# Optimization experiments

Measured on AMD Instinct MI355X. Metric: run time of the kernel, lower is better.

## Reference

```python
import jax, jax.numpy as jnp
import numpy as np

NH = 16      # num_heads
D = 128      # head_dim
C = 64       # chunk_size
EPS = 1e-12  # F.normalize eps


def setup_inputs() -> dict:
    key = jax.random.key(0)
    ks = jax.random.split(key, 12)
    B, L, H = 4, 4096, 2048
    std = 0.02
    f32 = jnp.float32
    inp = {
        "hidden_states": jax.random.normal(ks[0], (B, L, H), f32),
        # torch nn.Linear weights are [out_features, in_features]
        "q_w": jax.random.normal(ks[1], (NH * D, H), f32) * std,
        "q_b": jnp.zeros((NH * D,), f32),
        "k_w": jax.random.normal(ks[2], (NH * D, H), f32) * std,
        "k_b": jnp.zeros((NH * D,), f32),
        "v_w": jax.random.normal(ks[3], (NH * D, H), f32) * std,
        "v_b": jnp.zeros((NH * D,), f32),
        "a_w": jax.random.normal(ks[4], (NH, H), f32) * std,
        "a_b": jnp.zeros((NH,), f32),
        "b_w": jax.random.normal(ks[5], (NH, H), f32) * std,
        "b_b": jnp.zeros((NH,), f32),
        "og_w": jax.random.normal(ks[6], (NH * D, H), f32) * std,  # no bias
        "o_w": jax.random.normal(ks[7], (H, NH * D), f32) * std,
        "o_b": jnp.zeros((H,), f32),
    }
    return inp


def _l2norm(x):
    n = jnp.linalg.norm(x, axis=-1, keepdims=True)
    return x / jnp.maximum(n, EPS)


def reference(hidden_states, q_w, q_b, k_w, k_b, v_w, v_b,
              a_w, a_b, b_w, b_b, og_w, o_w, o_b):
    B, L, H = hidden_states.shape
    nh, d, c = NH, D, C
    hs = hidden_states

    q = (hs @ q_w.T + q_b).reshape(B, L, nh, d)
    k = (hs @ k_w.T + k_b).reshape(B, L, nh, d)
    v = (hs @ v_w.T + v_b).reshape(B, L, nh, d)
    # alpha = sigmoid(hs @ a_w.T + a_b) is computed in the original module but
    # never affects the output (alpha_mean / log_alpha are dead code) -> omitted.
    beta = jax.nn.softplus(hs @ b_w.T + b_b)            # [B,L,nh]

    scale = float(d) ** 0.5
    qn = _l2norm(q / scale)                              # normalize makes /scale moot, kept faithful
    kn = _l2norm(k / scale)
    gv = beta[..., None] * v                             # [B,L,nh,d]

    nchunks = L // c

    def to_chunks(x):  # [B,L,nh,d] -> [B,nchunks,nh,c,d]
        return x.reshape(B, nchunks, c, nh, d).transpose(0, 1, 3, 2, 4)

    qc, kc, gvc = to_chunks(qn), to_chunks(kn), to_chunks(gv)

    attn = jnp.einsum('bnhid,bnhjd->bnhij', qc, kc)      # per-chunk QK^T
    pos = jnp.arange(c, dtype=jnp.float32)
    dist = jnp.clip(pos[None, :] - pos[:, None], 0.0, None)   # (j-i) clamped >=0
    decay = jnp.exp(-0.1 * dist)
    causal = pos[None, :] <= pos[:, None]                # keep j<=i, zero j>i
    mask = jnp.where(causal, decay, 0.0)                 # [c,c]
    out = jnp.einsum('bnhij,bnhjd->bnhid', attn * mask, gvc)

    out = out.transpose(0, 1, 3, 2, 4).reshape(B, L, nh * d)
    gate = jax.nn.silu(hs @ og_w.T)                      # output_gate has no bias
    out = out * gate
    return out @ o_w.T + o_b
```

## Files before the change

kernel.cpp:

```cpp
#include <hip/hip_runtime.h>


typedef __bf16 bf16x8 __attribute__((ext_vector_type(8)));
typedef float f32x4 __attribute__((ext_vector_type(4)));

typedef __attribute__((address_space(1))) const unsigned int g_u32;
typedef __attribute__((address_space(3))) unsigned int l_u32;

__device__ __forceinline__ void cp16(const unsigned short* g, unsigned short* l) {
  __builtin_amdgcn_global_load_lds((g_u32*)g, (l_u32*)l, 16, 0, 0);
}

__device__ __forceinline__ unsigned short f2bf(float x) {
  unsigned u = __builtin_bit_cast(unsigned, x);
  u += 0x7fffu + ((u >> 16) & 1u);
  return (unsigned short)(u >> 16);
}
__device__ __forceinline__ float bf2f(unsigned short h) {
  return __builtin_bit_cast(float, (unsigned)h << 16);
}
__device__ __forceinline__ unsigned pk2(float a, float b) {
  return (unsigned)f2bf(a) | ((unsigned)f2bf(b) << 16);
}

__global__ __launch_bounds__(256) void cvt_bf16(const float* __restrict__ in,
                                                unsigned short* __restrict__ out,
                                                int n) {
  int i = (blockIdx.x * 256 + threadIdx.x) * 8;
  if (i >= n) return;
  float4 f0 = *(const float4*)(in + i);
  float4 f1 = *(const float4*)(in + i + 4);
  uint4 u;
  u.x = pk2(f0.x, f0.y); u.y = pk2(f0.z, f0.w);
  u.z = pk2(f1.x, f1.y); u.w = pk2(f1.z, f1.w);
  *(uint4*)(out + i) = u;
}

__global__ __launch_bounds__(256) void build_bias(
    const float* __restrict__ qb, const float* __restrict__ kb,
    const float* __restrict__ vb, float* __restrict__ bias_cat) {
  int i = blockIdx.x * 256 + threadIdx.x;
  float v = 0.f;
  if (i < 2048) v = qb[i];
  else if (i < 4096) v = kb[i - 2048];
  else if (i < 6144) v = vb[i - 4096];
  bias_cat[i] = v;
}

__global__ __launch_bounds__(256) void beta_kernel(
    const float* __restrict__ hs, const float* __restrict__ bw,
    const float* __restrict__ bb, float* __restrict__ beta,
    unsigned short* __restrict__ hsb) {
  __shared__ float row[2048];
  __shared__ float part[16][17];
  const int m = blockIdx.x;
  const float* src = hs + (size_t)m * 2048;
  for (int i = threadIdx.x; i < 512; i += 256)
    ((float4*)row)[i] = ((const float4*)src)[i];
  __syncthreads();
  if (hsb) {
    int e = threadIdx.x * 8;
    uint4 u;
    u.x = pk2(row[e], row[e + 1]);     u.y = pk2(row[e + 2], row[e + 3]);
    u.z = pk2(row[e + 4], row[e + 5]); u.w = pk2(row[e + 6], row[e + 7]);
    *(uint4*)(hsb + (size_t)m * 2048 + e) = u;
  }
  const int h = threadIdx.x >> 4, j = threadIdx.x & 15;
  const float* w = bw + h * 2048;
  float s = 0.f;
  #pragma unroll 8
  for (int kk = 0; kk < 128; kk++) {
    int k = j + (kk << 4);
    s += row[k] * w[k];
  }
  part[h][j] = s;
  __syncthreads();
  if (threadIdx.x < 16) {
    int hh = threadIdx.x;
    float t = bb[hh];
    #pragma unroll
    for (int j2 = 0; j2 < 16; j2++) t += part[hh][j2];
    beta[(size_t)m * 16 + hh] = fmaxf(t, 0.f) + log1pf(__expf(-fabsf(t)));
  }
}

template <int EPI, int N, int K>
__global__ __launch_bounds__(512, 2) void gemm256(
    const unsigned short* __restrict__ A, const unsigned short* __restrict__ Bw,
    const float* __restrict__ bias, const float* __restrict__ beta,
    void* __restrict__ Cv) {
  constexpr int NT = K / 32;
  __shared__ __align__(16) unsigned short As[4 * 8192];
  __shared__ __align__(16) unsigned short Bs[4 * 8192];
  const int tid = threadIdx.x;
  const int m0 = blockIdx.y * 256;
  const int n0 = blockIdx.x * 256;
  const int wid = tid >> 6, lane = tid & 63;
  const int wm = wid >> 2, wn = wid & 3;
  const int quad = lane >> 4, l16 = lane & 15;

  const int trow = tid >> 2;
  const int tch = (((tid & 3) ^ ((trow >> 1) & 3)) << 3);
  const unsigned short* Ag = A + (size_t)(m0 + trow) * K + tch;
  const unsigned short* Bg = Bw + (size_t)(n0 + trow) * K + tch;

  const int chs = ((quad ^ ((l16 >> 1) & 3)) << 4);
  const int a_lane = (wm * 128 + l16) * 64 + chs;
  const int b_lane = (wn * 64 + l16) * 64 + chs;

  f32x4 acc[8][4] = {};

  #pragma unroll
  for (int tt = 0; tt < 3; ++tt) {
    const size_t kk = (size_t)tt * 32;
    unsigned short* la = As + tt * 8192 + tid * 8;
    unsigned short* lb = Bs + tt * 8192 + tid * 8;
    cp16(Ag + kk, la);
    cp16(Ag + (size_t)128 * K + kk, la + 4096);
    cp16(Bg + kk, lb);
    cp16(Bg + (size_t)128 * K + kk, lb + 4096);
  }
  asm volatile("s_waitcnt vmcnt(8)" ::: "memory");
  __builtin_amdgcn_s_barrier();

  for (int t = 0; t < NT; ++t) {
    const int cur = t & 3;
    const int nb = (t + 3) & 3;
    const size_t k3 = (size_t)((t + 3 < NT) ? (t + 3) : (NT - 1)) * 32;
    const char* At = (const char*)As + cur * 16384 + a_lane;
    const char* Bt = (const char*)Bs + cur * 16384 + b_lane;
    unsigned short* la = As + nb * 8192 + tid * 8;
    unsigned short* lb = Bs + nb * 8192 + tid * 8;

    bf16x8 af[4], bfr[4];

    #pragma unroll
    for (int mi = 0; mi < 4; mi++) af[mi] = *(const bf16x8*)(At + mi * 1024);
    #pragma unroll
    for (int ni = 0; ni < 4; ni++) bfr[ni] = *(const bf16x8*)(Bt + ni * 1024);
    cp16(Ag + k3, la);
    cp16(Ag + (size_t)128 * K + k3, la + 4096);
    __builtin_amdgcn_s_barrier();
    asm volatile("s_waitcnt lgkmcnt(0)" ::: "memory");
    __builtin_amdgcn_s_setprio(1);
    #pragma unroll
    for (int mi = 0; mi < 4; mi++)
      #pragma unroll
      for (int ni = 0; ni < 4; ni++)
        acc[mi][ni] = __builtin_amdgcn_mfma_f32_16x16x32_bf16(
            af[mi], bfr[ni], acc[mi][ni], 0, 0, 0);
    __builtin_amdgcn_s_setprio(0);
    __builtin_amdgcn_s_barrier();

    #pragma unroll
    for (int mi = 0; mi < 4; mi++) af[mi] = *(const bf16x8*)(At + (4 + mi) * 1024);
    cp16(Bg + k3, lb);
    cp16(Bg + (size_t)128 * K + k3, lb + 4096);
    __builtin_amdgcn_s_barrier();
    asm volatile("s_waitcnt lgkmcnt(0)" ::: "memory");
    __builtin_amdgcn_s_setprio(1);
    #pragma unroll
    for (int mi = 0; mi < 4; mi++)
      #pragma unroll
      for (int ni = 0; ni < 4; ni++)
        acc[4 + mi][ni] = __builtin_amdgcn_mfma_f32_16x16x32_bf16(
            af[mi], bfr[ni], acc[4 + mi][ni], 0, 0, 0);
    __builtin_amdgcn_s_setprio(0);

    if (t != NT - 1) {
      asm volatile("s_waitcnt vmcnt(8)" ::: "memory");
      __builtin_amdgcn_s_barrier();
    }
  }
  asm volatile("s_waitcnt vmcnt(0)" ::: "memory");

  if (EPI == 0) {
    const int mode = n0 >> 11;
    unsigned short* outp =
        (unsigned short*)Cv + (size_t)mode * ((size_t)16384 * 2048);
    const int head = ((n0 + wn * 64) >> 7) & 15;
    #pragma unroll
    for (int mi = 0; mi < 8; mi++) {
      #pragma unroll
      for (int r = 0; r < 4; r++) {
        const int row = m0 + wm * 128 + mi * 16 + quad * 4 + r;
        const float bsc = (mode == 2) ? beta[(size_t)row * 16 + head] : 1.f;
        #pragma unroll
        for (int ni = 0; ni < 4; ni++) {
          const int col = n0 + wn * 64 + ni * 16 + l16;
          float x = acc[mi][ni][r] + bias[col];
          if (mode == 2) x *= bsc;
          if (mode == 3) x = x / (1.f + __expf(-x));
          outp[(size_t)row * 2048 + (col & 2047)] = f2bf(x);
        }
      }
    }
  } else {
    #pragma unroll
    for (int mi = 0; mi < 8; mi++)
      #pragma unroll
      for (int r = 0; r < 4; r++) {
        const int row = m0 + wm * 128 + mi * 16 + quad * 4 + r;
        #pragma unroll
        for (int ni = 0; ni < 4; ni++) {
          const int col = n0 + wn * 64 + ni * 16 + l16;
          ((float*)Cv)[(size_t)row * N + col] = acc[mi][ni][r] + bias[col];
        }
      }
  }
}

constexpr int GLDW = 40;
template <int EPI, bool ABF16>
__global__ __launch_bounds__(256) void gemm_bt(
    const void* __restrict__ Av, const float* __restrict__ Bw,
    const float* __restrict__ bias, const float* __restrict__ beta,
    void* __restrict__ Cv, int M, int N, int K) {
  __shared__ unsigned short As[128 * GLDW];
  __shared__ unsigned short Bs[128 * GLDW];
  const int tid = threadIdx.x;
  const int m0 = blockIdx.y * 128;
  const int n0 = blockIdx.x * 128;
  const int wid = tid >> 6, lane = tid & 63;
  const int wm = wid >> 1, wn = wid & 1;
  const int quad = lane >> 4, l16 = lane & 15;
  const int srow = tid >> 1, skh = (tid & 1) << 4;

  f32x4 acc[4][4] = {};
  const float* Bg = Bw + (size_t)(n0 + srow) * K + skh;

  for (int kb = 0; kb < K; kb += 32) {
    if (ABF16) {
      const unsigned short* Ag =
          (const unsigned short*)Av + (size_t)(m0 + srow) * K + kb + skh;
      uint4 u0 = ((const uint4*)Ag)[0];
      uint4 u1 = ((const uint4*)Ag)[1];
      uint4* d = (uint4*)&As[srow * GLDW + skh];
      d[0] = u0; d[1] = u1;
    } else {
      const float* Ag = (const float*)Av + (size_t)(m0 + srow) * K + kb + skh;
      float4 f0 = ((const float4*)Ag)[0];
      float4 f1 = ((const float4*)Ag)[1];
      float4 f2 = ((const float4*)Ag)[2];
      float4 f3 = ((const float4*)Ag)[3];
      unsigned* d = (unsigned*)&As[srow * GLDW + skh];
      d[0] = pk2(f0.x, f0.y); d[1] = pk2(f0.z, f0.w);
      d[2] = pk2(f1.x, f1.y); d[3] = pk2(f1.z, f1.w);
      d[4] = pk2(f2.x, f2.y); d[5] = pk2(f2.z, f2.w);
      d[6] = pk2(f3.x, f3.y); d[7] = pk2(f3.z, f3.w);
    }
    {
      const float* Bgk = Bg + kb;
      float4 f0 = ((const float4*)Bgk)[0];
      float4 f1 = ((const float4*)Bgk)[1];
      float4 f2 = ((const float4*)Bgk)[2];
      float4 f3 = ((const float4*)Bgk)[3];
      unsigned* d = (unsigned*)&Bs[srow * GLDW + skh];
      d[0] = pk2(f0.x, f0.y); d[1] = pk2(f0.z, f0.w);
      d[2] = pk2(f1.x, f1.y); d[3] = pk2(f1.z, f1.w);
      d[4] = pk2(f2.x, f2.y); d[5] = pk2(f2.z, f2.w);
      d[6] = pk2(f3.x, f3.y); d[7] = pk2(f3.z, f3.w);
    }
    __syncthreads();
    bf16x8 af[4], bfr[4];
    #pragma unroll
    for (int mi = 0; mi < 4; mi++)
      af[mi] = *(const bf16x8*)&As[(wm * 64 + mi * 16 + l16) * GLDW + (quad << 3)];
    #pragma unroll
    for (int ni = 0; ni < 4; ni++)
      bfr[ni] = *(const bf16x8*)&Bs[(wn * 64 + ni * 16 + l16) * GLDW + (quad << 3)];
    #pragma unroll
    for (int mi = 0; mi < 4; mi++)
      #pragma unroll
      for (int ni = 0; ni < 4; ni++)
        acc[mi][ni] = __builtin_amdgcn_mfma_f32_16x16x32_bf16(
            af[mi], bfr[ni], acc[mi][ni], 0, 0, 0);
    __syncthreads();
  }

  #pragma unroll
  for (int mi = 0; mi < 4; mi++) {
    #pragma unroll
    for (int r = 0; r < 4; r++) {
      const int row = m0 + wm * 64 + mi * 16 + quad * 4 + r;
      float bsc = 1.f;
      if (EPI == 1) bsc = beta[(size_t)row * 16 + blockIdx.x];
      #pragma unroll
      for (int ni = 0; ni < 4; ni++) {
        const int col = n0 + wn * 64 + ni * 16 + l16;
        float x = acc[mi][ni][r];
        if (EPI != 2) x += bias[col];
        if (EPI == 1) x *= bsc;
        if (EPI == 2) x = x / (1.f + __expf(-x));
        if (EPI == 3)
          ((float*)Cv)[(size_t)row * N + col] = x;
        else
          ((unsigned short*)Cv)[(size_t)row * N + col] = f2bf(x);
      }
    }
  }
}

constexpr int QK_LDW = 132;
constexpr int GT_LDW = 66;
constexpr int SS_LDW = 68;

__global__ __launch_bounds__(256) void attn_kernel(
    const unsigned short* __restrict__ qn, const unsigned short* __restrict__ kn,
    const unsigned short* __restrict__ gvp, const unsigned short* __restrict__ gate,
    unsigned short* __restrict__ y) {
  __shared__ unsigned short qs[64 * QK_LDW];
  __shared__ unsigned short ks[64 * QK_LDW];
  __shared__ unsigned short gst[128 * GT_LDW];
  __shared__ unsigned short Ss[64 * SS_LDW];

  const int tid = threadIdx.x;
  const int m0 = blockIdx.x * 64;
  const int h = blockIdx.y;
  const size_t gbase = (size_t)m0 * 2048 + (size_t)h * 128;

  #pragma unroll
  for (int it = 0; it < 4; it++) {
    int e = tid + it * 256;
    int i = e >> 4;
    int c = (e & 15) << 3;
    size_t g = gbase + (size_t)i * 2048 + c;
    *(uint4*)&qs[i * QK_LDW + c] = *(const uint4*)&qn[g];
    *(uint4*)&ks[i * QK_LDW + c] = *(const uint4*)&kn[g];
    uint4 gvv = *(const uint4*)&gvp[g];
    unsigned short tmp[8];
    *(uint4*)tmp = gvv;
    #pragma unroll
    for (int t = 0; t < 8; t++) gst[(c + t) * GT_LDW + i] = tmp[t];
  }
  __syncthreads();

  {
    const int rr = tid >> 2;
    const int seg = (tid & 3) * 32;
    float ssq = 0.f, ssk = 0.f;
    #pragma unroll
    for (int k2 = 0; k2 < 32; k2 += 2) {
      unsigned uq = *(const unsigned*)&qs[rr * QK_LDW + seg + k2];
      unsigned uk = *(const unsigned*)&ks[rr * QK_LDW + seg + k2];
      float a = bf2f((unsigned short)(uq & 0xffff)), b = bf2f((unsigned short)(uq >> 16));
      float c2 = bf2f((unsigned short)(uk & 0xffff)), d2 = bf2f((unsigned short)(uk >> 16));
      ssq += a * a + b * b;
      ssk += c2 * c2 + d2 * d2;
    }
    ssq += __shfl_xor(ssq, 1); ssq += __shfl_xor(ssq, 2);
    ssk += __shfl_xor(ssk, 1); ssk += __shfl_xor(ssk, 2);
    float iq = rsqrtf(fmaxf(ssq, 1e-24f));
    float ik = rsqrtf(fmaxf(ssk, 1e-24f));
    #pragma unroll
    for (int k2 = 0; k2 < 32; k2 += 2) {
      unsigned uq = *(const unsigned*)&qs[rr * QK_LDW + seg + k2];
      unsigned uk = *(const unsigned*)&ks[rr * QK_LDW + seg + k2];
      float a = bf2f((unsigned short)(uq & 0xffff)), b = bf2f((unsigned short)(uq >> 16));
      float c2 = bf2f((unsigned short)(uk & 0xffff)), d2 = bf2f((unsigned short)(uk >> 16));
      *(unsigned*)&qs[rr * QK_LDW + seg + k2] = pk2(a * iq, b * iq);
      *(unsigned*)&ks[rr * QK_LDW + seg + k2] = pk2(c2 * ik, d2 * ik);
    }
  }
  __syncthreads();

  const int w = tid >> 6;
  const int lane = tid & 63;
  const int quad = lane >> 4, l16 = lane & 15;

  {
    f32x4 acc[4] = {};
    #pragma unroll
    for (int kst = 0; kst < 4; kst++) {
      bf16x8 a = *(const bf16x8*)&qs[(w * 16 + l16) * QK_LDW + kst * 32 + (quad << 3)];
      #pragma unroll
      for (int ni = 0; ni < 4; ni++) {
        bf16x8 b = *(const bf16x8*)&ks[(ni * 16 + l16) * QK_LDW + kst * 32 + (quad << 3)];
        acc[ni] = __builtin_amdgcn_mfma_f32_16x16x32_bf16(a, b, acc[ni], 0, 0, 0);
      }
    }
    #pragma unroll
    for (int ni = 0; ni < 4; ni++)
      #pragma unroll
      for (int r = 0; r < 4; r++) {
        int row = w * 16 + quad * 4 + r;
        int col = ni * 16 + l16;
        float val = (col <= row) ? acc[ni][r] : 0.f;
        Ss[row * SS_LDW + col] = f2bf(val);
      }
  }
  __syncthreads();

  {
    f32x4 acc[8] = {};
    #pragma unroll
    for (int kst = 0; kst < 2; kst++) {
      bf16x8 a = *(const bf16x8*)&Ss[(w * 16 + l16) * SS_LDW + kst * 32 + (quad << 3)];
      #pragma unroll
      for (int nd = 0; nd < 8; nd++) {
        bf16x8 b = *(const bf16x8*)&gst[(nd * 16 + l16) * GT_LDW + kst * 32 + (quad << 3)];
        acc[nd] = __builtin_amdgcn_mfma_f32_16x16x32_bf16(a, b, acc[nd], 0, 0, 0);
      }
    }
    #pragma unroll
    for (int nd = 0; nd < 8; nd++)
      #pragma unroll
      for (int r = 0; r < 4; r++) {
        int row = w * 16 + quad * 4 + r;
        int col = nd * 16 + l16;
        size_t g = gbase + (size_t)row * 2048 + col;
        float gt = bf2f(gate[g]);
        y[g] = f2bf(acc[nd][r] * gt);
      }
  }
}

extern "C" void kernel_launch(void* const* d_in, const int* in_sizes, int n_in,
                              void* d_out, int out_size, void* d_ws, size_t ws_size,
                              hipStream_t stream) {
  const float* hs   = (const float*)d_in[0];
  const float* q_w  = (const float*)d_in[1];
  const float* q_b  = (const float*)d_in[2];
  const float* k_w  = (const float*)d_in[3];
  const float* k_b  = (const float*)d_in[4];
  const float* v_w  = (const float*)d_in[5];
  const float* v_b  = (const float*)d_in[6];
  const float* b_w  = (const float*)d_in[9];
  const float* b_b  = (const float*)d_in[10];
  const float* og_w = (const float*)d_in[11];
  const float* o_w  = (const float*)d_in[12];
  const float* o_b  = (const float*)d_in[13];

  const int M = 16384, K = 2048;
  const size_t MB64 = 67108864;

  const size_t OFF_HSB  = 4 * MB64;
  const size_t OFF_WCAT = OFF_HSB + MB64;
  const size_t OFF_OWB  = OFF_WCAT + 33554432;
  const size_t OFF_BETA = OFF_OWB + 8388608;
  const size_t OFF_BIAS = OFF_BETA + 1048576;
  const size_t NEED     = OFF_BIAS + 32768;

  char* ws = (char*)d_ws;

  if (ws_size >= NEED) {
    unsigned short* qy   = (unsigned short*)ws;
    unsigned short* knb  = (unsigned short*)(ws + MB64);
    unsigned short* gv   = (unsigned short*)(ws + 2 * MB64);
    unsigned short* gate = (unsigned short*)(ws + 3 * MB64);
    unsigned short* hsb  = (unsigned short*)(ws + OFF_HSB);
    unsigned short* wcat = (unsigned short*)(ws + OFF_WCAT);
    unsigned short* owb  = (unsigned short*)(ws + OFF_OWB);
    float*          beta = (float*)(ws + OFF_BETA);
    float*          bias = (float*)(ws + OFF_BIAS);

    const int NW = 4194304;
    cvt_bf16<<<NW / 2048, 256, 0, stream>>>(q_w,  wcat,          NW);
    cvt_bf16<<<NW / 2048, 256, 0, stream>>>(k_w,  wcat + NW,     NW);
    cvt_bf16<<<NW / 2048, 256, 0, stream>>>(v_w,  wcat + 2 * NW, NW);
    cvt_bf16<<<NW / 2048, 256, 0, stream>>>(og_w, wcat + 3 * NW, NW);
    cvt_bf16<<<NW / 2048, 256, 0, stream>>>(o_w,  owb,           NW);
    build_bias<<<32, 256, 0, stream>>>(q_b, k_b, v_b, bias);
    beta_kernel<<<M, 256, 0, stream>>>(hs, b_w, b_b, beta, hsb);

    gemm256<0, 8192, 2048><<<dim3(32, 64), 512, 0, stream>>>(
        hsb, wcat, bias, beta, qy);

    attn_kernel<<<dim3(256, 16), 256, 0, stream>>>(qy, knb, gv, gate, qy);

    gemm256<3, 2048, 2048><<<dim3(8, 64), 512, 0, stream>>>(
        qy, owb, o_b, nullptr, (float*)d_out);
  } else {
    unsigned short* qy   = (unsigned short*)ws;
    unsigned short* knb  = (unsigned short*)(ws + MB64);
    unsigned short* gv   = (unsigned short*)(ws + 2 * MB64);
    unsigned short* gate = (unsigned short*)(ws + 3 * MB64);
    float*          beta = (float*)(ws + 4 * MB64);

    beta_kernel<<<M, 256, 0, stream>>>(hs, b_w, b_b, beta, nullptr);
    dim3 gg(16, 128);
    gemm_bt<0, false><<<gg, 256, 0, stream>>>(hs, q_w, q_b, nullptr, qy, M, 2048, K);
    gemm_bt<0, false><<<gg, 256, 0, stream>>>(hs, k_w, k_b, nullptr, knb, M, 2048, K);
    gemm_bt<1, false><<<gg, 256, 0, stream>>>(hs, v_w, v_b, beta, gv, M, 2048, K);
    gemm_bt<2, false><<<gg, 256, 0, stream>>>(hs, og_w, nullptr, nullptr, gate, M, 2048, K);
    attn_kernel<<<dim3(256, 16), 256, 0, stream>>>(qy, knb, gv, gate, qy);
    gemm_bt<3, true><<<gg, 256, 0, stream>>>(qy, o_w, o_b, nullptr, (float*)d_out, M, 2048, K);
  }
}
```

Baseline: 1.296 ms.

## Restructure GEMM mainloop to K=64 double-buffered quadrant schedule

The 256x256 GEMM mainloop moves from a 4-stage ring of K=32 tiles to a 2-buffer scheme with K=64 tiles. Each K-step is split into four MFMA quadrant phases, and register fragments (aL/aH, bX/bY) are reused across phases. Global-to-LDS copies for the next tiles are interleaved between phases, and the LDS swizzle is changed to 8-chunk XOR. The aim is fewer barriers and LDS reads per MFMA and better overlap of loads with compute, at the cost of more fragment registers and a trickier wait/barrier ordering that could introduce races.

```diff
diff --git a/kernel.cpp b/kernel.cpp
--- a/kernel.cpp
+++ b/kernel.cpp
@@ -89,9 +89,9 @@
     const unsigned short* __restrict__ A, const unsigned short* __restrict__ Bw,
     const float* __restrict__ bias, const float* __restrict__ beta,
     void* __restrict__ Cv) {
-  constexpr int NT = K / 32;
-  __shared__ __align__(16) unsigned short As[4 * 8192];
-  __shared__ __align__(16) unsigned short Bs[4 * 8192];
+  constexpr int NT = K / 64;
+  static_assert(NT >= 3, "pipeline needs >=3 K-steps");
+  __shared__ __align__(16) unsigned short S[2 * 32768];
   const int tid = threadIdx.x;
   const int m0 = blockIdx.y * 256;
   const int n0 = blockIdx.x * 256;
@@ -99,78 +99,119 @@
   const int wm = wid >> 2, wn = wid & 3;
   const int quad = lane >> 4, l16 = lane & 15;
 
-  const int trow = tid >> 2;
-  const int tch = (((tid & 3) ^ ((trow >> 1) & 3)) << 3);
-  const unsigned short* Ag = A + (size_t)(m0 + trow) * K + tch;
-  const unsigned short* Bg = Bw + (size_t)(n0 + trow) * K + tch;
-
-  const int chs = ((quad ^ ((l16 >> 1) & 3)) << 4);
-  const int a_lane = (wm * 128 + l16) * 64 + chs;
-  const int b_lane = (wn * 64 + l16) * 64 + chs;
+  const int sidx = tid >> 3;
+  const int sc = tid & 7;
+  const int scol = ((sc ^ (sidx & 7)) << 3);
+  const unsigned short* pA = A + (size_t)(m0 + sidx) * K + scol;
+  const int rbx = ((sidx >> 5) << 6) + (sidx & 31);
+  const unsigned short* pB = Bw + (size_t)(n0 + rbx) * K + scol;
+
+  auto STG = [&](int roff , const unsigned short* src) {
+    cp16(src, S + roff + tid * 8);
+    cp16(src + (size_t)128 * K, S + roff + 4096 + tid * 8);
+  };
+
+  const int sig = l16 & 7;
+  const int ck0 = ((quad ^ sig) << 4);
+  const int ck1 = (((4 + quad) ^ sig) << 4);
+  const int aro = (wm * 64 + l16) * 128;
+  const int bro = (wn * 32 + l16) * 128;
 
   f32x4 acc[8][4] = {};
-
-  #pragma unroll
-  for (int tt = 0; tt < 3; ++tt) {
-    const size_t kk = (size_t)tt * 32;
-    unsigned short* la = As + tt * 8192 + tid * 8;
-    unsigned short* lb = Bs + tt * 8192 + tid * 8;
-    cp16(Ag + kk, la);
-    cp16(Ag + (size_t)128 * K + kk, la + 4096);
-    cp16(Bg + kk, lb);
-    cp16(Bg + (size_t)128 * K + kk, lb + 4096);
-  }
-  asm volatile("s_waitcnt vmcnt(8)" ::: "memory");
+  bf16x8 aL[4][2], aH[4][2], bX[2][2], bY[2][2];
+
+  STG(0,             pA);
+  STG(8192,          pA + (size_t)64 * K);
+  STG(16384,         pB);
+  STG(24576,         pB + (size_t)32 * K);
+  STG(32768,         pA + 64);
+  STG(32768 + 16384, pB + 64);
+  STG(32768 + 24576, pB + (size_t)32 * K + 64);
+  asm volatile("s_waitcnt vmcnt(6)" ::: "memory");
   __builtin_amdgcn_s_barrier();
 
   for (int t = 0; t < NT; ++t) {
-    const int cur = t & 3;
-    const int nb = (t + 3) & 3;
-    const size_t k3 = (size_t)((t + 3 < NT) ? (t + 3) : (NT - 1)) * 32;
-    const char* At = (const char*)As + cur * 16384 + a_lane;
-    const char* Bt = (const char*)Bs + cur * 16384 + b_lane;
-    unsigned short* la = As + nb * 8192 + tid * 8;
-    unsigned short* lb = Bs + nb * 8192 + tid * 8;
-
-    bf16x8 af[4], bfr[4];
-
-    #pragma unroll
-    for (int mi = 0; mi < 4; mi++) af[mi] = *(const bf16x8*)(At + mi * 1024);
-    #pragma unroll
-    for (int ni = 0; ni < 4; ni++) bfr[ni] = *(const bf16x8*)(Bt + ni * 1024);
-    cp16(Ag + k3, la);
-    cp16(Ag + (size_t)128 * K + k3, la + 4096);
-    __builtin_amdgcn_s_barrier();
-    asm volatile("s_waitcnt lgkmcnt(0)" ::: "memory");
+    const int cur = (t & 1) << 15;
+    const int nxt = 32768 - cur;
+    const char* B0 = (const char*)S + cur * 2;
+    const int koff1 = (t + 1 < NT ? t + 1 : NT - 1) * 64;
+    const int koff2 = (t + 2 < NT ? t + 2 : NT - 1) * 64;
+
+    #pragma unroll
+    for (int mi = 0; mi < 4; mi++) {
+      aL[mi][0] = *(const bf16x8*)(B0 + aro + mi * 2048 + ck0);
+      aL[mi][1] = *(const bf16x8*)(B0 + aro + mi * 2048 + ck1);
+    }
+    #pragma unroll
+    for (int ni = 0; ni < 2; ni++) {
+      bX[ni][0] = *(const bf16x8*)(B0 + 32768 + bro + ni * 2048 + ck0);
+      bX[ni][1] = *(const bf16x8*)(B0 + 32768 + bro + ni * 2048 + ck1);
+    }
+    STG(nxt + 8192, pA + (size_t)64 * K + koff1);
+    __builtin_amdgcn_s_barrier();
     __builtin_amdgcn_s_setprio(1);
     #pragma unroll
-    for (int mi = 0; mi < 4; mi++)
-      #pragma unroll
-      for (int ni = 0; ni < 4; ni++)
-        acc[mi][ni] = __builtin_amdgcn_mfma_f32_16x16x32_bf16(
-            af[mi], bfr[ni], acc[mi][ni], 0, 0, 0);
+    for (int k = 0; k < 2; k++)
+      #pragma unroll
+      for (int mi = 0; mi < 4; mi++)
+        #pragma unroll
+        for (int ni = 0; ni < 2; ni++)
+          acc[mi][ni] = __builtin_amdgcn_mfma_f32_16x16x32_bf16(
+              aL[mi][k], bX[ni][k], acc[mi][ni], 0, 0, 0);
     __builtin_amdgcn_s_setprio(0);
     __builtin_amdgcn_s_barrier();
 
     #pragma unroll
-    for (int mi = 0; mi < 4; mi++) af[mi] = *(const bf16x8*)(At + (4 + mi) * 1024);
-    cp16(Bg + k3, lb);
-    cp16(Bg + (size_t)128 * K + k3, lb + 4096);
-    __builtin_amdgcn_s_barrier();
-    asm volatile("s_waitcnt lgkmcnt(0)" ::: "memory");
+    for (int ni = 0; ni < 2; ni++) {
+      bY[ni][0] = *(const bf16x8*)(B0 + 49152 + bro + ni * 2048 + ck0);
+      bY[ni][1] = *(const bf16x8*)(B0 + 49152 + bro + ni * 2048 + ck1);
+    }
+    STG(cur, pA + koff2);
+    __builtin_amdgcn_s_barrier();
     __builtin_amdgcn_s_setprio(1);
     #pragma unroll
-    for (int mi = 0; mi < 4; mi++)
-      #pragma unroll
-      for (int ni = 0; ni < 4; ni++)
-        acc[4 + mi][ni] = __builtin_amdgcn_mfma_f32_16x16x32_bf16(
-            af[mi], bfr[ni], acc[4 + mi][ni], 0, 0, 0);
+    for (int k = 0; k < 2; k++)
+      #pragma unroll
+      for (int mi = 0; mi < 4; mi++)
+        #pragma unroll
+        for (int ni = 0; ni < 2; ni++)
+          acc[mi][2 + ni] = __builtin_amdgcn_mfma_f32_16x16x32_bf16(
+              aL[mi][k], bY[ni][k], acc[mi][2 + ni], 0, 0, 0);
     __builtin_amdgcn_s_setprio(0);
-
-    if (t != NT - 1) {
-      asm volatile("s_waitcnt vmcnt(8)" ::: "memory");
-      __builtin_amdgcn_s_barrier();
-    }
+    __builtin_amdgcn_s_barrier();
+
+    #pragma unroll
+    for (int mi = 0; mi < 4; mi++) {
+      aH[mi][0] = *(const bf16x8*)(B0 + 16384 + aro + mi * 2048 + ck0);
+      aH[mi][1] = *(const bf16x8*)(B0 + 16384 + aro + mi * 2048 + ck1);
+    }
+    STG(cur + 16384, pB + koff2);
+    __builtin_amdgcn_s_barrier();
+    __builtin_amdgcn_s_setprio(1);
+    #pragma unroll
+    for (int k = 0; k < 2; k++)
+      #pragma unroll
+      for (int mi = 0; mi < 4; mi++)
+        #pragma unroll
+        for (int ni = 0; ni < 2; ni++)
+          acc[4 + mi][2 + ni] = __builtin_amdgcn_mfma_f32_16x16x32_bf16(
+              aH[mi][k], bY[ni][k], acc[4 + mi][2 + ni], 0, 0, 0);
+    __builtin_amdgcn_s_setprio(0);
+    __builtin_amdgcn_s_barrier();
+
+    STG(cur + 24576, pB + (size_t)32 * K + koff2);
+    __builtin_amdgcn_s_setprio(1);
+    #pragma unroll
+    for (int k = 0; k < 2; k++)
+      #pragma unroll
+      for (int mi = 0; mi < 4; mi++)
+        #pragma unroll
+        for (int ni = 0; ni < 2; ni++)
+          acc[4 + mi][ni] = __builtin_amdgcn_mfma_f32_16x16x32_bf16(
+              aH[mi][k], bX[ni][k], acc[4 + mi][ni], 0, 0, 0);
+    __builtin_amdgcn_s_setprio(0);
+    asm volatile("s_waitcnt vmcnt(6)" ::: "memory");
+    __builtin_amdgcn_s_barrier();
   }
   asm volatile("s_waitcnt vmcnt(0)" ::: "memory");
 
```

After: 1.137 ms. -12.3%, faster.
